# Kernel tuning notes

Hardware: AMD Instinct MI355X
Metric: run time of the kernel (lower is better)

Reference implementation:

```python
import jax, jax.numpy as jnp
import numpy as np

B, S, HID = 2, 4096, 1024
NH, HD = 16, 64
R = 2  # dilation_rate


def setup_inputs() -> dict:
    key = jax.random.key(0)
    ks = jax.random.split(key, 6)
    sc = 0.02
    return {
        "hidden_states": jax.random.normal(ks[0], (B, S, HID), jnp.float32),
        "Wq": jax.random.normal(ks[1], (HID, HID), jnp.float32) * sc,
        "Wk": jax.random.normal(ks[2], (HID, HID), jnp.float32) * sc,
        "Wv": jax.random.normal(ks[3], (HID, HID), jnp.float32) * sc,
        "Wo": jax.random.normal(ks[4], (HID, HID), jnp.float32) * sc,
        "bo": jnp.zeros((HID,), jnp.float32),
    }


def reference(hidden_states, Wq, Wk, Wv, Wo, bo):
    bsz, q_len, _ = hidden_states.shape
    # projections (torch Linear: y = x @ W.T)
    q = jnp.einsum('bsh,oh->bso', hidden_states, Wq).reshape(bsz, q_len, NH, HD).transpose(0, 2, 1, 3)
    k = jnp.einsum('bsh,oh->bso', hidden_states, Wk).reshape(bsz, q_len, NH, HD).transpose(0, 2, 1, 3)
    v = jnp.einsum('bsh,oh->bso', hidden_states, Wv).reshape(bsz, q_len, NH, HD).transpose(0, 2, 1, 3)
    # strided dilation gather (indices 0, R, 2R, ...)
    q = q[:, :, ::R, :]
    k = k[:, :, ::R, :]
    v = v[:, :, ::R, :]
    sd = q.shape[2]  # dilated length
    # SDPA with is_causal=True over the dilated subsequence
    scores = jnp.einsum('bhqd,bhkd->bhqk', q, k) / np.sqrt(HD).astype(np.float32)
    causal = jnp.tril(jnp.ones((sd, sd), bool))
    scores = jnp.where(causal, scores, jnp.finfo(scores.dtype).min)
    probs = jax.nn.softmax(scores, axis=-1)
    attn = jnp.einsum('bhqk,bhkd->bhqd', probs, v)  # [B, H, sd, HD]
    attn = attn.transpose(0, 2, 1, 3).reshape(bsz, sd, HID)
    # scatter back into zero-initialized full-length tensor
    full = jnp.zeros((bsz, q_len, HID), attn.dtype).at[:, ::R, :].set(attn)
    return jnp.einsum('bsh,oh->bso', full, Wo) + bo
```

## Files before the change

kernel.cpp:

```cpp
#include <hip/hip_runtime.h>
#include <cstdint>

typedef unsigned short u16;
typedef unsigned int u32;
typedef __attribute__((ext_vector_type(8))) short short8;
typedef __attribute__((ext_vector_type(4))) float f32x4;
typedef __attribute__((ext_vector_type(4))) unsigned short u16x4;

#define S_ 4096
#define SD 2048

__device__ __forceinline__ u16 f2bf(float f) {
  union { float f; u32 u; } v; v.f = f;
  u32 r = v.u + 0x7fffu + ((v.u >> 16) & 1u);
  return (u16)(r >> 16);
}
__device__ __forceinline__ u32 pk2bf(float a, float b) {
  union { float f; u32 u; } ua, ub; ua.f = a; ub.f = b;
  return __builtin_amdgcn_perm(ub.u + 0x8000u, ua.u + 0x8000u, 0x07060302u);
}
__device__ __forceinline__ f32x4 mfma16(short8 a, short8 b, f32x4 c) {
  return __builtin_amdgcn_mfma_f32_16x16x32_bf16(a, b, c, 0, 0, 0);
}
__device__ __forceinline__ void async16(const void* g, void* l) {
  __builtin_amdgcn_global_load_lds((__attribute__((address_space(1))) void*)g,
                                   (__attribute__((address_space(3))) void*)l,
                                   16, 0, 0);
}

__global__ __launch_bounds__(256) void cast_all(const float* __restrict__ hs,
                                                const float* __restrict__ Wq,
                                                const float* __restrict__ Wk,
                                                const float* __restrict__ Wv,
                                                const float* __restrict__ Wo,
                                                u16* __restrict__ dstW,
                                                u16* __restrict__ dstX) {
  int bid = blockIdx.x;
  if (bid < 4096) {
    int gid = bid * 256 + threadIdx.x;
    int wsel = gid >> 18;
    int off  = (gid & 262143) * 4;
    const float* src = (wsel == 0) ? Wq : (wsel == 1) ? Wk : (wsel == 2) ? Wv : Wo;
    float scl = (wsel == 0) ? 0.18033688f : 1.0f;
    f32x4 v = *(const f32x4*)(src + off);
    u16x4 o; o.x = f2bf(v.x * scl); o.y = f2bf(v.y * scl);
    o.z = f2bf(v.z * scl); o.w = f2bf(v.w * scl);
    *(u16x4*)(dstW + (size_t)wsel * 1048576 + off) = o;
  } else {
    int gid = (bid - 4096) * 256 + threadIdx.x;
    int e = gid * 4;
    int m = e >> 10, col = e & 1023;
    int b = m >> 11, sm = m & 2047;
    const float* src = hs + ((size_t)(b * S_ + 2 * sm) << 10) + col;
    f32x4 v = *(const f32x4*)src;
    u16x4 o; o.x = f2bf(v.x); o.y = f2bf(v.y); o.z = f2bf(v.z); o.w = f2bf(v.w);
    *(u16x4*)(dstX + ((size_t)m << 10) + col) = o;
  }
}

__device__ __forceinline__ void gemm_body128(const u16* __restrict__ A,
                                             const u16* __restrict__ B,
                                             u16* __restrict__ C, int N,
                                             int bm, int bn, char* lA, char* lB) {
  const int tid = threadIdx.x, lane = tid & 63, w = tid >> 6;
  const int quad = lane >> 4, l15 = lane & 15;
  const int wm = (w & 1) * 64, wn = (w >> 1) * 64;
  f32x4 acc[4][4] = {};

  auto stage = [&](int buf, int k0) {
#pragma unroll
    for (int i = 0; i < 2; i++) {
      int p = i * 256 + tid;
      int row = p >> 2, cp = p & 3;
      int c = cp ^ ((row ^ (row >> 2)) & 3);
      async16(A + (size_t)(bm + row) * 1024 + k0 + c * 8,
              lA + buf * 8192 + i * 4096 + w * 1024);
      async16(B + (size_t)(bn + row) * 1024 + k0 + c * 8,
              lB + buf * 8192 + i * 4096 + w * 1024);
    }
  };

  stage(0, 0);
#pragma unroll 1
  for (int kt = 0; kt < 32; kt++) {
    __syncthreads();
    if (kt + 1 < 32) stage((kt + 1) & 1, (kt + 1) * 32);
    const char* A_ = lA + (kt & 1) * 8192;
    const char* B_ = lB + (kt & 1) * 8192;
    short8 af[4], bf[4];
#pragma unroll
    for (int mi = 0; mi < 4; mi++) {
      int row = wm + mi * 16 + l15;
      af[mi] = *(const short8*)(A_ + (row * 4 + (quad ^ ((row ^ (row >> 2)) & 3))) * 16);
    }
#pragma unroll
    for (int ni = 0; ni < 4; ni++) {
      int row = wn + ni * 16 + l15;
      bf[ni] = *(const short8*)(B_ + (row * 4 + (quad ^ ((row ^ (row >> 2)) & 3))) * 16);
    }
#pragma unroll
    for (int mi = 0; mi < 4; mi++)
#pragma unroll
      for (int ni = 0; ni < 4; ni++)
        acc[mi][ni] = mfma16(af[mi], bf[ni], acc[mi][ni]);
  }
#pragma unroll
  for (int mi = 0; mi < 4; mi++)
#pragma unroll
    for (int ni = 0; ni < 4; ni++) {
      int m0 = bm + wm + mi * 16 + quad * 4;
      int n = bn + wn + ni * 16 + l15;
#pragma unroll
      for (int r = 0; r < 4; r++)
        C[(size_t)(m0 + r) * N + n] = f2bf(acc[mi][ni][r]);
    }
}

__global__ __launch_bounds__(256) void qkv_gemm(const u16* __restrict__ X,
                                                const u16* __restrict__ Wbf,
                                                u16* __restrict__ QK,
                                                u16* __restrict__ Vt) {
  __shared__ __align__(16) char lA[16384];
  __shared__ __align__(16) char lB[16384];
  int bid = blockIdx.x;
  if (bid < 512) {
    gemm_body128(X, Wbf, QK, 2048, (bid >> 4) * 128, (bid & 15) * 128, lA, lB);
  } else {
    int b2 = bid - 512;
    gemm_body128(Wbf + 2 * 1048576, X, Vt, 4096, (b2 >> 5) * 128, (b2 & 31) * 128, lA, lB);
  }
}

__global__ __launch_bounds__(256) void oproj(const u16* __restrict__ A,
                                             const u16* __restrict__ B,
                                             const float* __restrict__ bo,
                                             float* __restrict__ out) {
  __shared__ __align__(16) char lA[2 * 4096];
  __shared__ __align__(16) char lB[2 * 8192];
  const int tid = threadIdx.x, lane = tid & 63, w = tid >> 6;
  const int quad = lane >> 4, l15 = lane & 15;
  const int bm = blockIdx.y * 64, bn = blockIdx.x * 128;
  const int wm = (w & 1) * 32, wn = (w >> 1) * 64;
  f32x4 acc[2][4] = {};

  auto stage = [&](int buf, int k0) {
    {
      int p = tid;
      int row = p >> 2, cp = p & 3;
      int c = cp ^ ((row ^ (row >> 2)) & 3);
      async16(A + (size_t)(bm + row) * 1024 + k0 + c * 8, lA + buf * 4096 + w * 1024);
    }
#pragma unroll
    for (int i = 0; i < 2; i++) {
      int p = i * 256 + tid;
      int row = p >> 2, cp = p & 3;
      int c = cp ^ ((row ^ (row >> 2)) & 3);
      async16(B + (size_t)(bn + row) * 1024 + k0 + c * 8, lB + buf * 8192 + i * 4096 + w * 1024);
    }
  };

  stage(0, 0);
#pragma unroll 1
  for (int kt = 0; kt < 32; kt++) {
    __syncthreads();
    if (kt + 1 < 32) stage((kt + 1) & 1, (kt + 1) * 32);
    const char* A_ = lA + (kt & 1) * 4096;
    const char* B_ = lB + (kt & 1) * 8192;
    short8 af[2], bf[4];
#pragma unroll
    for (int mi = 0; mi < 2; mi++) {
      int row = wm + mi * 16 + l15;
      af[mi] = *(const short8*)(A_ + (row * 4 + (quad ^ ((row ^ (row >> 2)) & 3))) * 16);
    }
#pragma unroll
    for (int ni = 0; ni < 4; ni++) {
      int row = wn + ni * 16 + l15;
      bf[ni] = *(const short8*)(B_ + (row * 4 + (quad ^ ((row ^ (row >> 2)) & 3))) * 16);
    }
#pragma unroll
    for (int mi = 0; mi < 2; mi++)
#pragma unroll
      for (int ni = 0; ni < 4; ni++)
        acc[mi][ni] = mfma16(af[mi], bf[ni], acc[mi][ni]);
  }
#pragma unroll
  for (int mi = 0; mi < 2; mi++)
#pragma unroll
    for (int ni = 0; ni < 4; ni++) {
      int n = bn + wn + ni * 16 + l15;
      float bias = bo[n];
#pragma unroll
      for (int r = 0; r < 4; r++) {
        int m = bm + wm + mi * 16 + quad * 4 + r;
        int bb = m >> 11, sm = m & 2047;
        size_t grow = ((size_t)(bb * S_ + 2 * sm)) << 10;
        out[grow + n] = acc[mi][ni][r] + bias;
        out[grow + 1024 + n] = bias;
      }
    }
}

__global__ __launch_bounds__(256) void attn3(const u16* __restrict__ QK,
                                             const u16* __restrict__ Vt,
                                             u16* __restrict__ O) {
  __shared__ __align__(16) char lK[2][8192];
  __shared__ __align__(16) char lV[2][8192];
  __shared__ __align__(16) char lP[4][2048];
  const int tid = threadIdx.x, lane = tid & 63, w = tid >> 6;
  const int quad = lane >> 4, l15 = lane & 15;
  const int h = blockIdx.x, b = blockIdx.y;
  const int qt = 31 - (int)blockIdx.z;
  const int qb = qt * 64 + w * 16;
  const int sw = l15 & 7;

  const u16* qp = QK + (size_t)(b * SD + qb + l15) * 2048 + h * 64 + quad * 8;
  short8 qf0 = *(const short8*)qp;
  short8 qf1 = *(const short8*)(qp + 32);

  auto stage = [&](int buf, int kb) {
#pragma unroll
    for (int i = 0; i < 2; i++) {
      int p = (w * 2 + i) * 64 + lane;
      int row = p >> 3, c = (p & 7) ^ (row & 7);
      async16(QK + (size_t)(b * SD + kb + row) * 2048 + 1024 + h * 64 + c * 8,
              lK[buf] + (w * 2 + i) * 1024);
      async16(Vt + (size_t)(h * 64 + row) * 4096 + b * SD + kb + c * 8,
              lV[buf] + (w * 2 + i) * 1024);
    }
  };

  f32x4 oacc[4] = {};
  float l4[4] = {0.f, 0.f, 0.f, 0.f};
  char* Pw = lP[w];

  stage(0, 0);
#pragma unroll 1
  for (int kt = 0; kt <= qt; kt++) {
    __syncthreads();
    if (kt + 1 <= qt) stage((kt + 1) & 1, (kt + 1) * 64);
    const char* K_ = lK[kt & 1];
    const char* V_ = lV[kt & 1];

    f32x4 s[4];
#pragma unroll
    for (int m = 0; m < 4; m++) {
      int key = m * 16 + l15;
      short8 kf0 = *(const short8*)(K_ + (key * 8 + (quad ^ (key & 7))) * 16);
      short8 kf1 = *(const short8*)(K_ + (key * 8 + ((4 + quad) ^ (key & 7))) * 16);
      f32x4 a = {};
      a = mfma16(kf0, qf0, a);
      a = mfma16(kf1, qf1, a);
      s[m] = a;
    }
    if (kt == qt) {
      int qrel = w * 16 + l15;
#pragma unroll
      for (int m = 0; m < 4; m++)
#pragma unroll
        for (int r = 0; r < 4; r++)
          if (m * 16 + quad * 4 + r > qrel) s[m][r] = -1e30f;
    }
    float pr[4][4];
#pragma unroll
    for (int m = 0; m < 4; m++) {
#pragma unroll
      for (int r = 0; r < 4; r++) pr[m][r] = exp2f(s[m][r]);
      l4[m] += (pr[m][0] + pr[m][1]) + (pr[m][2] + pr[m][3]);
    }
#pragma unroll
    for (int m = 0; m < 4; m++) {
      int c = m * 2 + (quad >> 1);
      int base = l15 * 128 + ((c ^ sw) * 16) + (quad & 1) * 8;
      *(u32*)(Pw + base)     = pk2bf(pr[m][0], pr[m][1]);
      *(u32*)(Pw + base + 4) = pk2bf(pr[m][2], pr[m][3]);
    }
    short8 pf0 = *(const short8*)(Pw + l15 * 128 + ((quad ^ sw) * 16));
    short8 pf1 = *(const short8*)(Pw + l15 * 128 + (((4 + quad) ^ sw) * 16));

#pragma unroll
    for (int m = 0; m < 4; m++) {
      int dim = m * 16 + l15;
      short8 vf0 = *(const short8*)(V_ + (dim * 8 + (quad ^ (dim & 7))) * 16);
      short8 vf1 = *(const short8*)(V_ + (dim * 8 + ((4 + quad) ^ (dim & 7))) * 16);
      oacc[m] = mfma16(vf0, pf0, oacc[m]);
      oacc[m] = mfma16(vf1, pf1, oacc[m]);
    }
  }
  float l = (l4[0] + l4[1]) + (l4[2] + l4[3]);
  l += __shfl_xor(l, 16, 64);
  l += __shfl_xor(l, 32, 64);
  float inv = 1.0f / l;
  u16* op = O + (size_t)(b * SD + qb + l15) * 1024 + h * 64;
#pragma unroll
  for (int m = 0; m < 4; m++) {
    u16x4 ov;
#pragma unroll
    for (int r = 0; r < 4; r++) ov[r] = f2bf(oacc[m][r] * inv);
    *(u16x4*)(op + m * 16 + quad * 4) = ov;
  }
}

extern "C" void kernel_launch(void* const* d_in, const int* in_sizes, int n_in,
                              void* d_out, int out_size, void* d_ws, size_t ws_size,
                              hipStream_t stream) {
  (void)in_sizes; (void)n_in; (void)out_size; (void)ws_size;
  const float* hs = (const float*)d_in[0];
  const float* Wq = (const float*)d_in[1];
  const float* Wk = (const float*)d_in[2];
  const float* Wv = (const float*)d_in[3];
  const float* Wo = (const float*)d_in[4];
  const float* bo = (const float*)d_in[5];
  float* out = (float*)d_out;
  char* ws = (char*)d_ws;

  u16* Xbf = (u16*)ws;
  u16* Wbf = (u16*)(ws + (8u << 20));
  u16* QKb = (u16*)(ws + (16u << 20));
  u16* Vtb = (u16*)(ws + (32u << 20));
  u16* Ob  = (u16*)(ws + (40u << 20));

  cast_all<<<8192, 256, 0, stream>>>(hs, Wq, Wk, Wv, Wo, Wbf, Xbf);
  qkv_gemm<<<768, 256, 0, stream>>>(Xbf, Wbf, QKb, Vtb);
  attn3<<<dim3(16, 2, 32), 256, 0, stream>>>(QKb, Vtb, Ob);
  oproj<<<dim3(8, 64), 256, 0, stream>>>(Ob, Wbf + 3 * 1048576, bo, out);
}
```

Before: 192.1 us.

## Shrink GEMM tiles, load V directly to registers, use hardware bf16 pack

The QKV GEMM tile goes from 128x128 to 128x64 and the output projection tile from 64x128 to 64x64, doubling the block count in each launch for better CU occupancy on the 256-CU part. In attention, V fragments are now read straight from global memory into registers each iteration instead of being staged through LDS, which frees LDS and removes those LDS reads. The P packing uses the hardware cvt_pk_bf16 builtin when it is available. Smaller tiles reduce data reuse per block and raise global traffic, and the direct V loads are not double-buffered, so their latency may be exposed.

```diff
diff --git a/kernel.cpp b/kernel.cpp
--- a/kernel.cpp
+++ b/kernel.cpp
@@ -15,10 +15,17 @@
   u32 r = v.u + 0x7fffu + ((v.u >> 16) & 1u);
   return (u16)(r >> 16);
 }
-__device__ __forceinline__ u32 pk2bf(float a, float b) {
+#if __has_builtin(__builtin_amdgcn_cvt_pk_bf16_f32)
+__device__ __forceinline__ u32 pkbf(float a, float b) {
+  auto r = __builtin_amdgcn_cvt_pk_bf16_f32(a, b);
+  u32 o; __builtin_memcpy(&o, &r, 4); return o;
+}
+#else
+__device__ __forceinline__ u32 pkbf(float a, float b) {
   union { float f; u32 u; } ua, ub; ua.f = a; ub.f = b;
   return __builtin_amdgcn_perm(ub.u + 0x8000u, ua.u + 0x8000u, 0x07060302u);
 }
+#endif
 __device__ __forceinline__ f32x4 mfma16(short8 a, short8 b, f32x4 c) {
   return __builtin_amdgcn_mfma_f32_16x16x32_bf16(a, b, c, 0, 0, 0);
 }
@@ -58,14 +65,26 @@
   }
 }
 
-__device__ __forceinline__ void gemm_body128(const u16* __restrict__ A,
-                                             const u16* __restrict__ B,
-                                             u16* __restrict__ C, int N,
-                                             int bm, int bn, char* lA, char* lB) {
+__global__ __launch_bounds__(256) void qkv_gemm(const u16* __restrict__ X,
+                                                const u16* __restrict__ Wbf,
+                                                u16* __restrict__ QK,
+                                                u16* __restrict__ Vt) {
+  __shared__ __align__(16) char lA[16384];
+  __shared__ __align__(16) char lB[8192];
   const int tid = threadIdx.x, lane = tid & 63, w = tid >> 6;
   const int quad = lane >> 4, l15 = lane & 15;
-  const int wm = (w & 1) * 64, wn = (w >> 1) * 64;
-  f32x4 acc[4][4] = {};
+  int bid = blockIdx.x;
+  const u16 *A, *B; u16* C; int N, bm, bn;
+  if (bid < 1024) {
+    A = X; B = Wbf; C = QK; N = 2048;
+    bm = (bid >> 5) * 128; bn = (bid & 31) * 64;
+  } else {
+    int b2 = bid - 1024;
+    A = Wbf + 2 * 1048576; B = X; C = Vt; N = 4096;
+    bm = (b2 >> 6) * 128; bn = (b2 & 63) * 64;
+  }
+  const int wm = (w & 1) * 64, wn = (w >> 1) * 32;
+  f32x4 acc[4][2] = {};
 
   auto stage = [&](int buf, int k0) {
 #pragma unroll
@@ -75,8 +94,13 @@
       int c = cp ^ ((row ^ (row >> 2)) & 3);
       async16(A + (size_t)(bm + row) * 1024 + k0 + c * 8,
               lA + buf * 8192 + i * 4096 + w * 1024);
+    }
+    {
+      int p = tid;
+      int row = p >> 2, cp = p & 3;
+      int c = cp ^ ((row ^ (row >> 2)) & 3);
       async16(B + (size_t)(bn + row) * 1024 + k0 + c * 8,
-              lB + buf * 8192 + i * 4096 + w * 1024);
+              lB + buf * 4096 + w * 1024);
     }
   };
 
@@ -86,77 +110,53 @@
     __syncthreads();
     if (kt + 1 < 32) stage((kt + 1) & 1, (kt + 1) * 32);
     const char* A_ = lA + (kt & 1) * 8192;
-    const char* B_ = lB + (kt & 1) * 8192;
-    short8 af[4], bf[4];
+    const char* B_ = lB + (kt & 1) * 4096;
+    short8 af[4], bf[2];
 #pragma unroll
     for (int mi = 0; mi < 4; mi++) {
       int row = wm + mi * 16 + l15;
       af[mi] = *(const short8*)(A_ + (row * 4 + (quad ^ ((row ^ (row >> 2)) & 3))) * 16);
     }
 #pragma unroll
-    for (int ni = 0; ni < 4; ni++) {
+    for (int ni = 0; ni < 2; ni++) {
       int row = wn + ni * 16 + l15;
       bf[ni] = *(const short8*)(B_ + (row * 4 + (quad ^ ((row ^ (row >> 2)) & 3))) * 16);
     }
 #pragma unroll
     for (int mi = 0; mi < 4; mi++)
 #pragma unroll
-      for (int ni = 0; ni < 4; ni++)
+      for (int ni = 0; ni < 2; ni++)
         acc[mi][ni] = mfma16(af[mi], bf[ni], acc[mi][ni]);
   }
 #pragma unroll
   for (int mi = 0; mi < 4; mi++)
 #pragma unroll
-    for (int ni = 0; ni < 4; ni++) {
+    for (int ni = 0; ni < 2; ni++) {
       int m0 = bm + wm + mi * 16 + quad * 4;
       int n = bn + wn + ni * 16 + l15;
 #pragma unroll
       for (int r = 0; r < 4; r++)
         C[(size_t)(m0 + r) * N + n] = f2bf(acc[mi][ni][r]);
     }
-}
-
-__global__ __launch_bounds__(256) void qkv_gemm(const u16* __restrict__ X,
-                                                const u16* __restrict__ Wbf,
-                                                u16* __restrict__ QK,
-                                                u16* __restrict__ Vt) {
-  __shared__ __align__(16) char lA[16384];
-  __shared__ __align__(16) char lB[16384];
-  int bid = blockIdx.x;
-  if (bid < 512) {
-    gemm_body128(X, Wbf, QK, 2048, (bid >> 4) * 128, (bid & 15) * 128, lA, lB);
-  } else {
-    int b2 = bid - 512;
-    gemm_body128(Wbf + 2 * 1048576, X, Vt, 4096, (b2 >> 5) * 128, (b2 & 31) * 128, lA, lB);
-  }
 }
 
 __global__ __launch_bounds__(256) void oproj(const u16* __restrict__ A,
                                              const u16* __restrict__ B,
                                              const float* __restrict__ bo,
                                              float* __restrict__ out) {
-  __shared__ __align__(16) char lA[2 * 4096];
-  __shared__ __align__(16) char lB[2 * 8192];
+  __shared__ __align__(16) char lA[8192];
+  __shared__ __align__(16) char lB[8192];
   const int tid = threadIdx.x, lane = tid & 63, w = tid >> 6;
   const int quad = lane >> 4, l15 = lane & 15;
-  const int bm = blockIdx.y * 64, bn = blockIdx.x * 128;
-  const int wm = (w & 1) * 32, wn = (w >> 1) * 64;
-  f32x4 acc[2][4] = {};
+  const int bm = blockIdx.y * 64, bn = blockIdx.x * 64;
+  const int wm = (w & 1) * 32, wn = (w >> 1) * 32;
+  f32x4 acc[2][2] = {};
 
   auto stage = [&](int buf, int k0) {
-    {
-      int p = tid;
-      int row = p >> 2, cp = p & 3;
-      int c = cp ^ ((row ^ (row >> 2)) & 3);
-      async16(A + (size_t)(bm + row) * 1024 + k0 + c * 8, lA + buf * 4096 + w * 1024);
-    }
-#pragma unroll
-    for (int i = 0; i < 2; i++) {
-      int p = i * 256 + tid;
-      int row = p >> 2, cp = p & 3;
-      int c = cp ^ ((row ^ (row >> 2)) & 3);
-      async16(B + (size_t)(bn + row) * 1024 + k0 + c * 8, lB + buf * 8192 + i * 4096 + w * 1024);
-    }
+    int row = tid >> 2, cp = tid & 3;
+    int c = cp ^ ((row ^ (row >> 2)) & 3);
+    async16(A + (size_t)(bm + row) * 1024 + k0 + c * 8, lA + buf * 4096 + w * 1024);
+    async16(B + (size_t)(bn + row) * 1024 + k0 + c * 8, lB + buf * 4096 + w * 1024);
   };
 
   stage(0, 0);
@@ -165,28 +165,28 @@
     __syncthreads();
     if (kt + 1 < 32) stage((kt + 1) & 1, (kt + 1) * 32);
     const char* A_ = lA + (kt & 1) * 4096;
-    const char* B_ = lB + (kt & 1) * 8192;
-    short8 af[2], bf[4];
+    const char* B_ = lB + (kt & 1) * 4096;
+    short8 af[2], bf[2];
 #pragma unroll
     for (int mi = 0; mi < 2; mi++) {
       int row = wm + mi * 16 + l15;
       af[mi] = *(const short8*)(A_ + (row * 4 + (quad ^ ((row ^ (row >> 2)) & 3))) * 16);
     }
 #pragma unroll
-    for (int ni = 0; ni < 4; ni++) {
+    for (int ni = 0; ni < 2; ni++) {
       int row = wn + ni * 16 + l15;
       bf[ni] = *(const short8*)(B_ + (row * 4 + (quad ^ ((row ^ (row >> 2)) & 3))) * 16);
     }
 #pragma unroll
     for (int mi = 0; mi < 2; mi++)
 #pragma unroll
-      for (int ni = 0; ni < 4; ni++)
+      for (int ni = 0; ni < 2; ni++)
         acc[mi][ni] = mfma16(af[mi], bf[ni], acc[mi][ni]);
   }
 #pragma unroll
   for (int mi = 0; mi < 2; mi++)
 #pragma unroll
-    for (int ni = 0; ni < 4; ni++) {
+    for (int ni = 0; ni < 2; ni++) {
       int n = bn + wn + ni * 16 + l15;
       float bias = bo[n];
 #pragma unroll
@@ -200,11 +200,10 @@
     }
 }
 
-__global__ __launch_bounds__(256) void attn3(const u16* __restrict__ QK,
+__global__ __launch_bounds__(256) void attn4(const u16* __restrict__ QK,
                                              const u16* __restrict__ Vt,
                                              u16* __restrict__ O) {
   __shared__ __align__(16) char lK[2][8192];
-  __shared__ __align__(16) char lV[2][8192];
   __shared__ __align__(16) char lP[4][2048];
   const int tid = threadIdx.x, lane = tid & 63, w = tid >> 6;
   const int quad = lane >> 4, l15 = lane & 15;
@@ -217,29 +216,35 @@
   short8 qf0 = *(const short8*)qp;
   short8 qf1 = *(const short8*)(qp + 32);
 
-  auto stage = [&](int buf, int kb) {
+  auto stageK = [&](int buf, int kb) {
 #pragma unroll
     for (int i = 0; i < 2; i++) {
       int p = (w * 2 + i) * 64 + lane;
       int row = p >> 3, c = (p & 7) ^ (row & 7);
       async16(QK + (size_t)(b * SD + kb + row) * 2048 + 1024 + h * 64 + c * 8,
               lK[buf] + (w * 2 + i) * 1024);
-      async16(Vt + (size_t)(h * 64 + row) * 4096 + b * SD + kb + c * 8,
-              lV[buf] + (w * 2 + i) * 1024);
     }
   };
 
   f32x4 oacc[4] = {};
   float l4[4] = {0.f, 0.f, 0.f, 0.f};
   char* Pw = lP[w];
-
-  stage(0, 0);
+  const u16* vbase = Vt + ((size_t)(h * 64 + l15)) * 4096 + b * SD + quad * 8;
+
+  stageK(0, 0);
 #pragma unroll 1
   for (int kt = 0; kt <= qt; kt++) {
+    const int kb = kt * 64;
     __syncthreads();
-    if (kt + 1 <= qt) stage((kt + 1) & 1, (kt + 1) * 64);
+    short8 vf0[4], vf1[4];
+#pragma unroll
+    for (int m = 0; m < 4; m++) {
+      const u16* vp = vbase + (size_t)(m * 16) * 4096 + kb;
+      vf0[m] = *(const short8*)vp;
+      vf1[m] = *(const short8*)(vp + 32);
+    }
+    if (kt + 1 <= qt) stageK((kt + 1) & 1, (kt + 1) * 64);
     const char* K_ = lK[kt & 1];
-    const char* V_ = lV[kt & 1];
 
     f32x4 s[4];
 #pragma unroll
@@ -271,19 +276,16 @@
     for (int m = 0; m < 4; m++) {
       int c = m * 2 + (quad >> 1);
       int base = l15 * 128 + ((c ^ sw) * 16) + (quad & 1) * 8;
-      *(u32*)(Pw + base)     = pk2bf(pr[m][0], pr[m][1]);
-      *(u32*)(Pw + base + 4) = pk2bf(pr[m][2], pr[m][3]);
+      *(u32*)(Pw + base)     = pkbf(pr[m][0], pr[m][1]);
+      *(u32*)(Pw + base + 4) = pkbf(pr[m][2], pr[m][3]);
     }
     short8 pf0 = *(const short8*)(Pw + l15 * 128 + ((quad ^ sw) * 16));
     short8 pf1 = *(const short8*)(Pw + l15 * 128 + (((4 + quad) ^ sw) * 16));
 
 #pragma unroll
     for (int m = 0; m < 4; m++) {
-      int dim = m * 16 + l15;
-      short8 vf0 = *(const short8*)(V_ + (dim * 8 + (quad ^ (dim & 7))) * 16);
-      short8 vf1 = *(const short8*)(V_ + (dim * 8 + ((4 + quad) ^ (dim & 7))) * 16);
-      oacc[m] = mfma16(vf0, pf0, oacc[m]);
-      oacc[m] = mfma16(vf1, pf1, oacc[m]);
+      oacc[m] = mfma16(vf0[m], pf0, oacc[m]);
+      oacc[m] = mfma16(vf1[m], pf1, oacc[m]);
     }
   }
   float l = (l4[0] + l4[1]) + (l4[2] + l4[3]);
@@ -320,7 +322,7 @@
   u16* Ob  = (u16*)(ws + (40u << 20));
 
   cast_all<<<8192, 256, 0, stream>>>(hs, Wq, Wk, Wv, Wo, Wbf, Xbf);
-  qkv_gemm<<<768, 256, 0, stream>>>(Xbf, Wbf, QKb, Vtb);
-  attn3<<<dim3(16, 2, 32), 256, 0, stream>>>(QKb, Vtb, Ob);
-  oproj<<<dim3(8, 64), 256, 0, stream>>>(Ob, Wbf + 3 * 1048576, bo, out);
-}
+  qkv_gemm<<<1536, 256, 0, stream>>>(Xbf, Wbf, QKb, Vtb);
+  attn4<<<dim3(16, 2, 32), 256, 0, stream>>>(QKb, Vtb, Ob);
+  oproj<<<dim3(16, 64), 256, 0, stream>>>(Ob, Wbf + 3 * 1048576, bo, out);
+}
```

New measurement: 229.6 us. +19.5%, slower.
